# Optimization experiments

Hardware: AMD Instinct MI355X
Metric: run time of the kernel (lower is better)

The kernel has to match this reference:

```python
import jax, jax.numpy as jnp
from jax import lax
import numpy as np

VOCAB = 50000
EMBED = 300
UNITS = 512          # num_nodes[0]
D1 = 1024            # num_nodes[1]
D2 = 1024            # num_nodes[2]
NUM_CLASSES = 20
B, T = 64, 512


def setup_inputs() -> dict:
    key = jax.random.key(0)
    ks = jax.random.split(key, 12)
    s = 0.02
    return {
        "tokens": jax.random.randint(ks[0], (B, T), 0, VOCAB),
        "emb": jax.random.normal(ks[1], (VOCAB, EMBED), jnp.float32) * s,
        "Wx": jax.random.normal(ks[2], (EMBED, 4 * UNITS), jnp.float32) * s,
        "Wh": jax.random.normal(ks[3], (UNITS, 4 * UNITS), jnp.float32) * s,
        "b": jnp.zeros((4 * UNITS,), jnp.float32),
        "W1": jax.random.normal(ks[4], (UNITS, D1), jnp.float32) * s,
        "b1": jnp.zeros((D1,), jnp.float32),
        "W2": jax.random.normal(ks[5], (D1, D2), jnp.float32) * s,
        "b2": jnp.zeros((D2,), jnp.float32),
        "Wo": jax.random.normal(ks[6], (D2, NUM_CLASSES), jnp.float32) * s,
        "bo": jnp.zeros((NUM_CLASSES,), jnp.float32),
    }


def reference(tokens, emb, Wx, Wh, b, W1, b1, W2, b2, Wo, bo):
    # Embedding with mask_zero=True: token 0 timesteps are masked -> LSTM skips
    # the state update (Keras semantics).
    mask = (tokens != 0)                               # [B, T]
    x = emb[tokens]                                    # [B, T, E]
    units = Wh.shape[0]
    # Precompute input contribution to the gates (parallel over time).
    xg = jnp.einsum('bte,eg->btg', x, Wx) + b          # [B, T, 4U]

    def step(carry, inp):
        h, c = carry
        g_x, m = inp                                   # [B,4U], [B]
        g = g_x + h @ Wh                               # [B, 4U]
        i, f, cc, o = jnp.split(g, 4, axis=-1)         # Keras gate order i,f,c,o
        i = jax.nn.sigmoid(i)
        f = jax.nn.sigmoid(f)
        o = jax.nn.sigmoid(o)
        # activation='relu' replaces tanh in candidate and output transform.
        c_new = f * c + i * jax.nn.relu(cc)
        h_new = o * jax.nn.relu(c_new)
        m = m[:, None]
        h = jnp.where(m, h_new, h)
        c = jnp.where(m, c_new, c)
        return (h, c), None

    h0 = jnp.zeros((tokens.shape[0], units), x.dtype)
    (h, _), _ = lax.scan(step, (h0, h0),
                         (jnp.swapaxes(xg, 0, 1), mask.T))  # scan over T

    h = jax.nn.relu(h @ W1 + b1)
    h = jax.nn.relu(h @ W2 + b2)
    return jax.nn.softmax(h @ Wo + bo)
```

## Files before the change

### kernel.cpp

```cpp
#include <hip/hip_runtime.h>
#include <hip/hip_bf16.h>

#define B_   64
#define T_   512
#define E_   300
#define U_   512
#define G4_  2048
#define D1_  1024
#define D2_  1024
#define NC_  20
#define KP_  320

typedef __bf16 bf16x8 __attribute__((ext_vector_type(8)));
typedef float  f32x4  __attribute__((ext_vector_type(4)));

__device__ __forceinline__ float sigmoidf_(float x) { return 1.0f / (1.0f + __expf(-x)); }

__device__ __forceinline__ void gl_lds16(const void* g, void* l) {
    __builtin_amdgcn_global_load_lds(
        (const __attribute__((address_space(1))) unsigned int*)g,
        (__attribute__((address_space(3))) unsigned int*)l, 16, 0, 0);
}

__global__ void init_kernel(unsigned int* __restrict__ hz, int* __restrict__ flags) {
    int idx = blockIdx.x * 256 + threadIdx.x;
    if (idx < (B_ * U_ / 2)) hz[idx] = 0u;
    if (idx < 256) flags[idx] = 0;
}

__global__ __launch_bounds__(256) void prep_wxT(const float* __restrict__ Wx,
                                                __hip_bfloat16* __restrict__ wxT) {
    __shared__ __hip_bfloat16 t[64][65];
    const int n0 = blockIdx.x * 64;
    const int k0 = blockIdx.y * 64;
    const int tid = threadIdx.x;
    for (int i = tid; i < 4096; i += 256) {
        int r = i >> 6, c = i & 63;
        int k = k0 + r;
        float v = (k < E_) ? Wx[(size_t)k * G4_ + n0 + c] : 0.f;
        t[r][c] = __float2bfloat16(v);
    }
    __syncthreads();
    for (int i = tid; i < 4096; i += 256) {
        int r = i >> 6, c = i & 63;
        wxT[(size_t)(n0 + r) * KP_ + k0 + c] = t[c][r];
    }
}

__global__ __launch_bounds__(256) void prep_xb(const int* __restrict__ tokens,
                                               const float* __restrict__ emb,
                                               __hip_bfloat16* __restrict__ xb) {
    const int row = blockIdx.x * 4 + (threadIdx.x >> 6);
    const int ln  = threadIdx.x & 63;
    const int tok = tokens[row];
    const float* src = emb + (size_t)tok * E_;
    __hip_bfloat16* dst = xb + (size_t)row * KP_;
    for (int k = ln; k < KP_; k += 64)
        dst[k] = (k < E_) ? __float2bfloat16(src[k]) : __float2bfloat16(0.f);
}

__global__ __launch_bounds__(256) void xg_gemm(const __hip_bfloat16* __restrict__ xb,
                                               const __hip_bfloat16* __restrict__ wxT,
                                               const float* __restrict__ bias,
                                               __hip_bfloat16* __restrict__ xg) {
    const int n0g = blockIdx.x * 128;
    const int bt0 = blockIdx.y * 128;
    const int tid = threadIdx.x;
    const int w   = tid >> 6;
    const int ln  = tid & 63;
    const int fn  = ln & 15;
    const int quad = ln >> 4;
    const int m0  = (w >> 1) * 64;
    const int n0w = (w & 1) * 64;

    __shared__ __align__(16) __hip_bfloat16 As[128 * 32];
    __shared__ __align__(16) __hip_bfloat16 Bs[128 * 32];

    f32x4 acc[4][4];
    #pragma unroll
    for (int im = 0; im < 4; ++im)
        #pragma unroll
        for (int in = 0; in < 4; ++in)
            acc[im][in] = (f32x4){0.f, 0.f, 0.f, 0.f};

    const __hip_bfloat16* ga = xb  + (size_t)(bt0 + w * 32 + (ln >> 2)) * KP_ + (ln & 3) * 8;
    const __hip_bfloat16* gb = wxT + (size_t)(n0g + w * 32 + (ln >> 2)) * KP_ + (ln & 3) * 8;

    for (int kt = 0; kt < KP_ / 32; ++kt) {
        gl_lds16(ga,             &As[(w * 32) * 32]);
        gl_lds16(ga + 16 * KP_,  &As[(w * 32 + 16) * 32]);
        gl_lds16(gb,             &Bs[(w * 32) * 32]);
        gl_lds16(gb + 16 * KP_,  &Bs[(w * 32 + 16) * 32]);
        ga += 32; gb += 32;
        __syncthreads();

        bf16x8 af[4], bf[4];
        #pragma unroll
        for (int im = 0; im < 4; ++im)
            af[im] = *(const bf16x8*)&As[(m0 + im * 16 + fn) * 32 + quad * 8];
        #pragma unroll
        for (int in = 0; in < 4; ++in)
            bf[in] = *(const bf16x8*)&Bs[(n0w + in * 16 + fn) * 32 + quad * 8];
        #pragma unroll
        for (int im = 0; im < 4; ++im)
            #pragma unroll
            for (int in = 0; in < 4; ++in)
                acc[im][in] = __builtin_amdgcn_mfma_f32_16x16x32_bf16(
                    af[im], bf[in], acc[im][in], 0, 0, 0);
        __syncthreads();
    }

    #pragma unroll
    for (int in = 0; in < 4; ++in) {
        const int n = n0g + n0w + in * 16 + fn;
        const float bv = bias[n];
        #pragma unroll
        for (int im = 0; im < 4; ++im) {
            #pragma unroll
            for (int r = 0; r < 4; ++r) {
                int m = bt0 + m0 + im * 16 + quad * 4 + r;
                int bb = m >> 9, tt = m & 511;
                xg[(size_t)(tt * B_ + bb) * G4_ + n] =
                    __float2bfloat16(acc[im][in][r] + bv);
            }
        }
    }
}

__global__ __launch_bounds__(256) void lstm_kernel(const __hip_bfloat16* __restrict__ xg,
                                                   const int* __restrict__ tokens,
                                                   const float* __restrict__ Wh,
                                                   __hip_bfloat16* __restrict__ hbuf,
                                                   int* __restrict__ flags) {
    const int tid  = threadIdx.x;
    const int lane = tid & 63;
    const int wave = tid >> 6;
    const int x  = blockIdx.x & 7;
    const int r_ = blockIdx.x >> 3;
    const int ub = x * 8 + (r_ & 7);
    const int g  = r_ >> 3;
    const int u0 = ub * 8;

    __shared__ __align__(16) __hip_bfloat16 whsT[32][520];
    __shared__ __align__(16) __hip_bfloat16 hs[16][520];
    __shared__ float gbuf[16][32];
    __shared__ unsigned mask_lds[16][16];

    for (int idx = tid; idx < 32 * 512; idx += 256) {
        int c = idx & 31, k = idx >> 5;
        int col = ((c >> 3) << 9) + u0 + (c & 7);
        whsT[c][k] = __float2bfloat16(Wh[(size_t)k * G4_ + col]);
    }
    {
        int m = tid >> 4, wi = tid & 15;
        const int4* tp = (const int4*)(tokens + (size_t)(g * 16 + m) * T_ + wi * 32);
        unsigned bits = 0;
        #pragma unroll
        for (int q = 0; q < 8; ++q) {
            int4 v = tp[q];
            bits |= (v.x != 0 ? 1u : 0u) << (q * 4 + 0);
            bits |= (v.y != 0 ? 1u : 0u) << (q * 4 + 1);
            bits |= (v.z != 0 ? 1u : 0u) << (q * 4 + 2);
            bits |= (v.w != 0 ? 1u : 0u) << (q * 4 + 3);
        }
        mask_lds[m][wi] = bits;
    }

    float c0 = 0.f, c1 = 0.f, h0 = 0.f, h1 = 0.f;
    int* gflags = flags + g * 64;

    const int fn   = lane & 15;
    const int quad = lane >> 4;
    const int fc   = wave * 16 + fn;
    const int fcol = ((fc >> 3) << 9) + u0 + (fc & 7);

    __syncthreads();

    for (int s = 0; s < T_; ++s) {
        float xv[4];
        if (wave < 2) {
            #pragma unroll
            for (int r = 0; r < 4; ++r)
                xv[r] = __bfloat162float(
                    xg[(size_t)(s * B_ + g * 16 + quad * 4 + r) * G4_ + fcol]);
        }

        if (s > 0) {
            if (tid < 64) {
                while (__hip_atomic_load(&gflags[tid], __ATOMIC_RELAXED,
                                         __HIP_MEMORY_SCOPE_AGENT) < s)
                    __builtin_amdgcn_s_sleep(2);
            }
            __syncthreads();
        }

        {
            const uint4* hp = (const uint4*)(hbuf + (size_t)((s & 1) * B_ + g * 16) * U_);
            uint4 t0, t1, t2, t3;
            asm volatile(
                "global_load_dwordx4 %0, %4, off sc0 sc1\n\t"
                "global_load_dwordx4 %1, %5, off sc0 sc1\n\t"
                "global_load_dwordx4 %2, %6, off sc0 sc1\n\t"
                "s_waitcnt vmcnt(0)\n\t"
                "global_load_dwordx4 %3, %7, off sc0 sc1\n\t"
                "s_waitcnt vmcnt(0)"
                : "=&v"(t0), "=&v"(t1), "=&v"(t2), "=&v"(t3)
                : "v"(hp + tid), "v"(hp + tid + 256), "v"(hp + tid + 512),
                  "v"(hp + tid + 768)
                : "memory");
            int i0 = tid;        *((uint4*)&hs[i0 >> 6][(i0 & 63) * 8]) = t0;
            int i1 = tid + 256;  *((uint4*)&hs[i1 >> 6][(i1 & 63) * 8]) = t1;
            int i2 = tid + 512;  *((uint4*)&hs[i2 >> 6][(i2 & 63) * 8]) = t2;
            int i3 = tid + 768;  *((uint4*)&hs[i3 >> 6][(i3 & 63) * 8]) = t3;
        }
        __syncthreads();

        if (wave < 2) {
            f32x4 acc;
            #pragma unroll
            for (int r = 0; r < 4; ++r) acc[r] = xv[r];
            const __hip_bfloat16* arow = &hs[fn][quad * 8];
            const __hip_bfloat16* brow = &whsT[fc][quad * 8];
            #pragma unroll
            for (int kk = 0; kk < 16; ++kk) {
                bf16x8 av = *(const bf16x8*)(arow + kk * 32);
                bf16x8 bv = *(const bf16x8*)(brow + kk * 32);
                acc = __builtin_amdgcn_mfma_f32_16x16x32_bf16(av, bv, acc, 0, 0, 0);
            }
            #pragma unroll
            for (int r = 0; r < 4; ++r)
                gbuf[quad * 4 + r][fc] = acc[r];
        }
        __syncthreads();

        if (tid < 64) {
            const int m  = tid >> 2;
            const int u2 = (tid & 3) << 1;
            float gi0 = sigmoidf_(gbuf[m][u2]),      gi1 = sigmoidf_(gbuf[m][u2 + 1]);
            float gf0 = sigmoidf_(gbuf[m][8 + u2]),  gf1 = sigmoidf_(gbuf[m][9 + u2]);
            float gc0 = gbuf[m][16 + u2],            gc1 = gbuf[m][17 + u2];
            float go0 = sigmoidf_(gbuf[m][24 + u2]), go1 = sigmoidf_(gbuf[m][25 + u2]);
            float cn0 = gf0 * c0 + gi0 * fmaxf(gc0, 0.f);
            float cn1 = gf1 * c1 + gi1 * fmaxf(gc1, 0.f);
            float hn0 = go0 * fmaxf(cn0, 0.f);
            float hn1 = go1 * fmaxf(cn1, 0.f);
            if ((mask_lds[m][s >> 5] >> (s & 31)) & 1u) {
                c0 = cn0; c1 = cn1; h0 = hn0; h1 = hn1;
            }
            __hip_bfloat162 hv;
            hv.x = __float2bfloat16(h0);
            hv.y = __float2bfloat16(h1);
            unsigned wv;
            __builtin_memcpy(&wv, &hv, 4);
            unsigned* dst = (unsigned*)hbuf +
                (((((s + 1) & 1) * B_ + g * 16 + m) * U_ + u0 + u2) >> 1);
            __hip_atomic_store(dst, wv, __ATOMIC_RELAXED, __HIP_MEMORY_SCOPE_AGENT);
        }
        __syncthreads();
        if (tid == 0)
            __hip_atomic_store(&gflags[ub], s + 1, __ATOMIC_RELAXED,
                               __HIP_MEMORY_SCOPE_AGENT);
    }
}

__global__ __launch_bounds__(256) void fc1_kernel(const __hip_bfloat16* __restrict__ h,
                                                  const float* __restrict__ W,
                                                  const float* __restrict__ bias,
                                                  float* __restrict__ y) {
    int b = blockIdx.x >> 2, ch = blockIdx.x & 3;
    __shared__ float xrow[U_];
    for (int i = threadIdx.x; i < U_; i += 256)
        xrow[i] = __bfloat162float(h[b * U_ + i]);
    __syncthreads();
    int n = ch * 256 + threadIdx.x;
    float acc = 0.f;
    #pragma unroll 4
    for (int k = 0; k < U_; ++k) acc = fmaf(xrow[k], W[(size_t)k * D1_ + n], acc);
    y[b * D1_ + n] = fmaxf(acc + bias[n], 0.f);
}

__global__ __launch_bounds__(256) void fc2_kernel(const float* __restrict__ x,
                                                  const float* __restrict__ W,
                                                  const float* __restrict__ bias,
                                                  float* __restrict__ y) {
    int b = blockIdx.x >> 2, ch = blockIdx.x & 3;
    __shared__ float xrow[D1_];
    for (int i = threadIdx.x; i < D1_; i += 256) xrow[i] = x[b * D1_ + i];
    __syncthreads();
    int n = ch * 256 + threadIdx.x;
    float acc = 0.f;
    #pragma unroll 4
    for (int k = 0; k < D1_; ++k) acc = fmaf(xrow[k], W[(size_t)k * D2_ + n], acc);
    y[b * D2_ + n] = fmaxf(acc + bias[n], 0.f);
}

__global__ __launch_bounds__(64) void out_kernel(const float* __restrict__ h2,
                                                 const float* __restrict__ Wo,
                                                 const float* __restrict__ bo,
                                                 float* __restrict__ out) {
    int b = blockIdx.x;
    __shared__ float xrow[D2_];
    __shared__ float lg[NC_];
    __shared__ float red[2];
    for (int i = threadIdx.x; i < D2_; i += 64) xrow[i] = h2[b * D2_ + i];
    __syncthreads();
    if (threadIdx.x < NC_) {
        float a = bo[threadIdx.x];
        for (int k = 0; k < D2_; ++k) a = fmaf(xrow[k], Wo[k * NC_ + threadIdx.x], a);
        lg[threadIdx.x] = a;
    }
    __syncthreads();
    if (threadIdx.x == 0) {
        float mx = lg[0];
        for (int c = 1; c < NC_; ++c) mx = fmaxf(mx, lg[c]);
        float sm = 0.f;
        for (int c = 0; c < NC_; ++c) sm += expf(lg[c] - mx);
        red[0] = mx; red[1] = 1.0f / sm;
    }
    __syncthreads();
    if (threadIdx.x < NC_)
        out[b * NC_ + threadIdx.x] = expf(lg[threadIdx.x] - red[0]) * red[1];
}

extern "C" void kernel_launch(void* const* d_in, const int* in_sizes, int n_in,
                              void* d_out, int out_size, void* d_ws, size_t ws_size,
                              hipStream_t stream) {
    const int*   tokens = (const int*)d_in[0];
    const float* emb    = (const float*)d_in[1];
    const float* Wx     = (const float*)d_in[2];
    const float* Wh     = (const float*)d_in[3];
    const float* b      = (const float*)d_in[4];
    const float* W1     = (const float*)d_in[5];
    const float* b1     = (const float*)d_in[6];
    const float* W2     = (const float*)d_in[7];
    const float* b2     = (const float*)d_in[8];
    const float* Wo     = (const float*)d_in[9];
    const float* bo     = (const float*)d_in[10];
    float* out = (float*)d_out;

    char* ws = (char*)d_ws;
    const size_t XG_BYTES   = (size_t)T_ * B_ * G4_ * 2;
    const size_t HBUF_BYTES = (size_t)2 * B_ * U_ * 2;
    __hip_bfloat16* xg   = (__hip_bfloat16*)ws;
    __hip_bfloat16* hbuf = (__hip_bfloat16*)(ws + XG_BYTES);
    int* flags           = (int*)(ws + XG_BYTES + HBUF_BYTES);
    char* p = ws + XG_BYTES + HBUF_BYTES + 1024;
    float* h1            = (float*)p;                 p += (size_t)B_ * D1_ * 4;
    float* h2            = (float*)p;                 p += (size_t)B_ * D2_ * 4;
    __hip_bfloat16* xb   = (__hip_bfloat16*)p;        p += (size_t)B_ * T_ * KP_ * 2;
    __hip_bfloat16* wxT  = (__hip_bfloat16*)p;

    init_kernel<<<64, 256, 0, stream>>>((unsigned int*)hbuf, flags);
    prep_wxT<<<dim3(32, 5), 256, 0, stream>>>(Wx, wxT);
    prep_xb<<<(B_ * T_) / 4, 256, 0, stream>>>(tokens, emb, xb);
    xg_gemm<<<dim3(16, 256), 256, 0, stream>>>(xb, wxT, b, xg);
    lstm_kernel<<<256, 256, 0, stream>>>(xg, tokens, Wh, hbuf, flags);
    fc1_kernel<<<256, 256, 0, stream>>>(hbuf, W1, b1, h1);
    fc2_kernel<<<256, 256, 0, stream>>>(h1, W2, b2, h2);
    out_kernel<<<64, 64, 0, stream>>>(h2, Wo, bo, out);
}
```

Before: 1.643 ms.

## Drop per-step block barriers in persistent LSTM and split MFMA accumulator chain

Each step now has every wave poll the inter-block flags itself, instead of one wave polling and then a block barrier. The trailing barrier before the flag publish is removed: wave 0 waits for its own h stores with s_waitcnt and then sets the flag directly. The h-load asm no longer waits between loads, and the 16-deep MFMA dependency chain is split into two independent accumulators that are summed at the end. The aim is to shorten per-step latency on the serial recurrence. The cost is more polling traffic, and correctness now depends on the flag ordering alone to protect the shared-memory buffers.

After: 2.025 ms. +23.2%, slower.

```diff
diff --git a/kernel.cpp b/kernel.cpp
--- a/kernel.cpp
+++ b/kernel.cpp
@@ -168,12 +168,16 @@
 
     float c0 = 0.f, c1 = 0.f, h0 = 0.f, h1 = 0.f;
     int* gflags = flags + g * 64;
+    volatile int* myflag = gflags + (tid & 63);
 
     const int fn   = lane & 15;
     const int quad = lane >> 4;
     const int fc   = wave * 16 + fn;
     const int fcol = ((fc >> 3) << 9) + u0 + (fc & 7);
 
+    const uint4* hp0 = (const uint4*)(hbuf + (size_t)(g * 16) * U_) + tid;
+    const uint4* hp1 = (const uint4*)(hbuf + (size_t)(B_ + g * 16) * U_) + tid;
+
     __syncthreads();
 
     for (int s = 0; s < T_; ++s) {
@@ -186,27 +190,22 @@
         }
 
         if (s > 0) {
-            if (tid < 64) {
-                while (__hip_atomic_load(&gflags[tid], __ATOMIC_RELAXED,
-                                         __HIP_MEMORY_SCOPE_AGENT) < s)
-                    __builtin_amdgcn_s_sleep(2);
-            }
-            __syncthreads();
+            while (__hip_atomic_load(&gflags[tid & 63], __ATOMIC_RELAXED,
+                                     __HIP_MEMORY_SCOPE_AGENT) < s)
+                __builtin_amdgcn_s_sleep(1);
         }
 
         {
-            const uint4* hp = (const uint4*)(hbuf + (size_t)((s & 1) * B_ + g * 16) * U_);
+            const uint4* hp = (s & 1) ? hp1 : hp0;
             uint4 t0, t1, t2, t3;
             asm volatile(
                 "global_load_dwordx4 %0, %4, off sc0 sc1\n\t"
                 "global_load_dwordx4 %1, %5, off sc0 sc1\n\t"
                 "global_load_dwordx4 %2, %6, off sc0 sc1\n\t"
-                "s_waitcnt vmcnt(0)\n\t"
                 "global_load_dwordx4 %3, %7, off sc0 sc1\n\t"
                 "s_waitcnt vmcnt(0)"
                 : "=&v"(t0), "=&v"(t1), "=&v"(t2), "=&v"(t3)
-                : "v"(hp + tid), "v"(hp + tid + 256), "v"(hp + tid + 512),
-                  "v"(hp + tid + 768)
+                : "v"(hp), "v"(hp + 256), "v"(hp + 512), "v"(hp + 768)
                 : "memory");
             int i0 = tid;        *((uint4*)&hs[i0 >> 6][(i0 & 63) * 8]) = t0;
             int i1 = tid + 256;  *((uint4*)&hs[i1 >> 6][(i1 & 63) * 8]) = t1;
@@ -216,20 +215,23 @@
         __syncthreads();
 
         if (wave < 2) {
-            f32x4 acc;
-            #pragma unroll
-            for (int r = 0; r < 4; ++r) acc[r] = xv[r];
+            f32x4 acc0, acc1;
+            #pragma unroll
+            for (int r = 0; r < 4; ++r) { acc0[r] = xv[r]; acc1[r] = 0.f; }
             const __hip_bfloat16* arow = &hs[fn][quad * 8];
             const __hip_bfloat16* brow = &whsT[fc][quad * 8];
             #pragma unroll
-            for (int kk = 0; kk < 16; ++kk) {
-                bf16x8 av = *(const bf16x8*)(arow + kk * 32);
-                bf16x8 bv = *(const bf16x8*)(brow + kk * 32);
-                acc = __builtin_amdgcn_mfma_f32_16x16x32_bf16(av, bv, acc, 0, 0, 0);
+            for (int kk = 0; kk < 8; ++kk) {
+                bf16x8 av0 = *(const bf16x8*)(arow + kk * 32);
+                bf16x8 bv0 = *(const bf16x8*)(brow + kk * 32);
+                acc0 = __builtin_amdgcn_mfma_f32_16x16x32_bf16(av0, bv0, acc0, 0, 0, 0);
+                bf16x8 av1 = *(const bf16x8*)(arow + (kk + 8) * 32);
+                bf16x8 bv1 = *(const bf16x8*)(brow + (kk + 8) * 32);
+                acc1 = __builtin_amdgcn_mfma_f32_16x16x32_bf16(av1, bv1, acc1, 0, 0, 0);
             }
             #pragma unroll
             for (int r = 0; r < 4; ++r)
-                gbuf[quad * 4 + r][fc] = acc[r];
+                gbuf[quad * 4 + r][fc] = acc0[r] + acc1[r];
         }
         __syncthreads();
 
@@ -255,12 +257,13 @@
             unsigned* dst = (unsigned*)hbuf +
                 (((((s + 1) & 1) * B_ + g * 16 + m) * U_ + u0 + u2) >> 1);
             __hip_atomic_store(dst, wv, __ATOMIC_RELAXED, __HIP_MEMORY_SCOPE_AGENT);
-        }
-        __syncthreads();
-        if (tid == 0)
-            __hip_atomic_store(&gflags[ub], s + 1, __ATOMIC_RELAXED,
-                               __HIP_MEMORY_SCOPE_AGENT);
-    }
+            asm volatile("s_waitcnt vmcnt(0)" ::: "memory");
+            if (tid == 0)
+                __hip_atomic_store(&gflags[ub], s + 1, __ATOMIC_RELAXED,
+                                   __HIP_MEMORY_SCOPE_AGENT);
+        }
+    }
+    (void)myflag;
 }
 
 __global__ __launch_bounds__(256) void fc1_kernel(const __hip_bfloat16* __restrict__ h,
```

## Replace per-step flag barrier with step-tagged hidden-state words and prefetch xg

Applied to the files above, without the earlier changes.

The per-block completion flags and the spin-wait on them are removed. Each hidden-state bf16 pair is now stored alongside its step number in one 8-byte word. Readers load the state directly and retry any 16-byte chunk whose tags do not match the current step. This removes the separate flag poll and one __syncthreads per step, and the input-gate values for step s+1 are prefetched during step s. In exchange the hidden-state buffer doubles in size, spinning becomes per-chunk, and correctness now depends on each 8-byte store being seen as a single unit.

Result: slower. 2.568 ms (+56.2%).

```diff
diff --git a/kernel.cpp b/kernel.cpp
--- a/kernel.cpp
+++ b/kernel.cpp
@@ -22,10 +22,16 @@
         (__attribute__((address_space(3))) unsigned int*)l, 16, 0, 0);
 }
 
-__global__ void init_kernel(unsigned int* __restrict__ hz, int* __restrict__ flags) {
+__device__ __forceinline__ uint4 cload4(const uint4* p) {
+    uint4 t;
+    asm volatile("global_load_dwordx4 %0, %1, off sc0 sc1\n\ts_waitcnt vmcnt(0)"
+                 : "=v"(t) : "v"(p) : "memory");
+    return t;
+}
+
+__global__ void init_kernel(uint4* __restrict__ hz) {
     int idx = blockIdx.x * 256 + threadIdx.x;
-    if (idx < (B_ * U_ / 2)) hz[idx] = 0u;
-    if (idx < 256) flags[idx] = 0;
+    hz[idx] = (uint4){0u, 0u, 0u, 0u};
 }
 
 __global__ __launch_bounds__(256) void prep_wxT(const float* __restrict__ Wx,
@@ -130,8 +136,7 @@
 __global__ __launch_bounds__(256) void lstm_kernel(const __hip_bfloat16* __restrict__ xg,
                                                    const int* __restrict__ tokens,
                                                    const float* __restrict__ Wh,
-                                                   __hip_bfloat16* __restrict__ hbuf,
-                                                   int* __restrict__ flags) {
+                                                   uint2* __restrict__ hbuf2) {
     const int tid  = threadIdx.x;
     const int lane = tid & 63;
     const int wave = tid >> 6;
@@ -167,7 +172,6 @@
     }
 
     float c0 = 0.f, c1 = 0.f, h0 = 0.f, h1 = 0.f;
-    int* gflags = flags + g * 64;
 
     const int fn   = lane & 15;
     const int quad = lane >> 4;
@@ -176,44 +180,65 @@
 
     __syncthreads();
 
+    float xvp[4];
+    if (wave < 2) {
+        #pragma unroll
+        for (int r = 0; r < 4; ++r)
+            xvp[r] = __bfloat162float(
+                xg[(size_t)(0 * B_ + g * 16 + quad * 4 + r) * G4_ + fcol]);
+    }
+
     for (int s = 0; s < T_; ++s) {
         float xv[4];
         if (wave < 2) {
             #pragma unroll
+            for (int r = 0; r < 4; ++r) xv[r] = xvp[r];
+        }
+
+        {
+            const uint4* hp = (const uint4*)(hbuf2 +
+                (size_t)((s & 1) * (B_ * 256) + (g * 16) * 256)) + tid;
+            uint4 t0, t1, t2, t3, t4, t5, t6, t7;
+            asm volatile(
+                "global_load_dwordx4 %0, %8,  off sc0 sc1\n\t"
+                "global_load_dwordx4 %1, %9,  off sc0 sc1\n\t"
+                "global_load_dwordx4 %2, %10, off sc0 sc1\n\t"
+                "global_load_dwordx4 %3, %11, off sc0 sc1\n\t"
+                "global_load_dwordx4 %4, %12, off sc0 sc1\n\t"
+                "global_load_dwordx4 %5, %13, off sc0 sc1\n\t"
+                "global_load_dwordx4 %6, %14, off sc0 sc1\n\t"
+                "global_load_dwordx4 %7, %15, off sc0 sc1\n\t"
+                "s_waitcnt vmcnt(0)"
+                : "=&v"(t0), "=&v"(t1), "=&v"(t2), "=&v"(t3),
+                  "=&v"(t4), "=&v"(t5), "=&v"(t6), "=&v"(t7)
+                : "v"(hp), "v"(hp + 256), "v"(hp + 512), "v"(hp + 768),
+                  "v"(hp + 1024), "v"(hp + 1280), "v"(hp + 1536), "v"(hp + 1792)
+                : "memory");
+
+            const unsigned tgt = (unsigned)s;
+            #define RETRY_(tt, pp) \
+                while (tt.y != tgt || tt.w != tgt) { \
+                    __builtin_amdgcn_s_sleep(1); tt = cload4(pp); }
+            RETRY_(t0, hp);        RETRY_(t1, hp + 256);
+            RETRY_(t2, hp + 512);  RETRY_(t3, hp + 768);
+            RETRY_(t4, hp + 1024); RETRY_(t5, hp + 1280);
+            RETRY_(t6, hp + 1536); RETRY_(t7, hp + 1792);
+            #undef RETRY_
+
+            #define HSW_(tt, k) { int u = tid + 256 * (k); \
+                *(uint2*)&hs[u >> 7][(u & 127) * 4] = (uint2){tt.x, tt.z}; }
+            HSW_(t0, 0) HSW_(t1, 1) HSW_(t2, 2) HSW_(t3, 3)
+            HSW_(t4, 4) HSW_(t5, 5) HSW_(t6, 6) HSW_(t7, 7)
+            #undef HSW_
+        }
+        __syncthreads();
+
+        if (wave < 2 && s + 1 < T_) {
+            #pragma unroll
             for (int r = 0; r < 4; ++r)
-                xv[r] = __bfloat162float(
-                    xg[(size_t)(s * B_ + g * 16 + quad * 4 + r) * G4_ + fcol]);
-        }
-
-        if (s > 0) {
-            if (tid < 64) {
-                while (__hip_atomic_load(&gflags[tid], __ATOMIC_RELAXED,
-                                         __HIP_MEMORY_SCOPE_AGENT) < s)
-                    __builtin_amdgcn_s_sleep(2);
-            }
-            __syncthreads();
-        }
-
-        {
-            const uint4* hp = (const uint4*)(hbuf + (size_t)((s & 1) * B_ + g * 16) * U_);
-            uint4 t0, t1, t2, t3;
-            asm volatile(
-                "global_load_dwordx4 %0, %4, off sc0 sc1\n\t"
-                "global_load_dwordx4 %1, %5, off sc0 sc1\n\t"
-                "global_load_dwordx4 %2, %6, off sc0 sc1\n\t"
-                "s_waitcnt vmcnt(0)\n\t"
-                "global_load_dwordx4 %3, %7, off sc0 sc1\n\t"
-                "s_waitcnt vmcnt(0)"
-                : "=&v"(t0), "=&v"(t1), "=&v"(t2), "=&v"(t3)
-                : "v"(hp + tid), "v"(hp + tid + 256), "v"(hp + tid + 512),
-                  "v"(hp + tid + 768)
-                : "memory");
-            int i0 = tid;        *((uint4*)&hs[i0 >> 6][(i0 & 63) * 8]) = t0;
-            int i1 = tid + 256;  *((uint4*)&hs[i1 >> 6][(i1 & 63) * 8]) = t1;
-            int i2 = tid + 512;  *((uint4*)&hs[i2 >> 6][(i2 & 63) * 8]) = t2;
-            int i3 = tid + 768;  *((uint4*)&hs[i3 >> 6][(i3 & 63) * 8]) = t3;
-        }
-        __syncthreads();
+                xvp[r] = __bfloat162float(
+                    xg[(size_t)((s + 1) * B_ + g * 16 + quad * 4 + r) * G4_ + fcol]);
+        }
 
         if (wave < 2) {
             f32x4 acc;
@@ -252,25 +277,29 @@
             hv.y = __float2bfloat16(h1);
             unsigned wv;
             __builtin_memcpy(&wv, &hv, 4);
-            unsigned* dst = (unsigned*)hbuf +
-                (((((s + 1) & 1) * B_ + g * 16 + m) * U_ + u0 + u2) >> 1);
-            __hip_atomic_store(dst, wv, __ATOMIC_RELAXED, __HIP_MEMORY_SCOPE_AGENT);
-        }
-        __syncthreads();
-        if (tid == 0)
-            __hip_atomic_store(&gflags[ub], s + 1, __ATOMIC_RELAXED,
-                               __HIP_MEMORY_SCOPE_AGENT);
-    }
-}
-
-__global__ __launch_bounds__(256) void fc1_kernel(const __hip_bfloat16* __restrict__ h,
+            uint2 val; val.x = wv; val.y = (unsigned)(s + 1);
+            uint2* dst = hbuf2 + (size_t)(((s + 1) & 1) * (B_ * 256) +
+                                          (g * 16 + m) * 256 + ub * 4 + (tid & 3));
+            asm volatile("global_store_dwordx2 %0, %1, off sc0 sc1"
+                         :: "v"(dst), "v"(val) : "memory");
+        }
+        __builtin_amdgcn_s_barrier();
+    }
+}
+
+__global__ __launch_bounds__(256) void fc1_kernel(const uint2* __restrict__ hb2,
                                                   const float* __restrict__ W,
                                                   const float* __restrict__ bias,
                                                   float* __restrict__ y) {
     int b = blockIdx.x >> 2, ch = blockIdx.x & 3;
     __shared__ float xrow[U_];
-    for (int i = threadIdx.x; i < U_; i += 256)
-        xrow[i] = __bfloat162float(h[b * U_ + i]);
+    for (int i = threadIdx.x; i < U_ / 2; i += 256) {
+        uint2 v = hb2[(size_t)b * 256 + i];
+        __hip_bfloat162 hv;
+        __builtin_memcpy(&hv, &v.x, 4);
+        xrow[2 * i]     = __bfloat162float(hv.x);
+        xrow[2 * i + 1] = __bfloat162float(hv.y);
+    }
     __syncthreads();
     int n = ch * 256 + threadIdx.x;
     float acc = 0.f;
@@ -340,22 +369,21 @@
 
     char* ws = (char*)d_ws;
     const size_t XG_BYTES   = (size_t)T_ * B_ * G4_ * 2;
-    const size_t HBUF_BYTES = (size_t)2 * B_ * U_ * 2;
-    __hip_bfloat16* xg   = (__hip_bfloat16*)ws;
-    __hip_bfloat16* hbuf = (__hip_bfloat16*)(ws + XG_BYTES);
-    int* flags           = (int*)(ws + XG_BYTES + HBUF_BYTES);
-    char* p = ws + XG_BYTES + HBUF_BYTES + 1024;
+    const size_t HB2_BYTES  = (size_t)2 * B_ * 256 * 8;
+    __hip_bfloat16* xg  = (__hip_bfloat16*)ws;
+    uint2* hbuf2        = (uint2*)(ws + XG_BYTES);
+    char* p = ws + XG_BYTES + HB2_BYTES;
     float* h1            = (float*)p;                 p += (size_t)B_ * D1_ * 4;
     float* h2            = (float*)p;                 p += (size_t)B_ * D2_ * 4;
     __hip_bfloat16* xb   = (__hip_bfloat16*)p;        p += (size_t)B_ * T_ * KP_ * 2;
     __hip_bfloat16* wxT  = (__hip_bfloat16*)p;
 
-    init_kernel<<<64, 256, 0, stream>>>((unsigned int*)hbuf, flags);
+    init_kernel<<<64, 256, 0, stream>>>((uint4*)hbuf2);
     prep_wxT<<<dim3(32, 5), 256, 0, stream>>>(Wx, wxT);
     prep_xb<<<(B_ * T_) / 4, 256, 0, stream>>>(tokens, emb, xb);
     xg_gemm<<<dim3(16, 256), 256, 0, stream>>>(xb, wxT, b, xg);
-    lstm_kernel<<<256, 256, 0, stream>>>(xg, tokens, Wh, hbuf, flags);
-    fc1_kernel<<<256, 256, 0, stream>>>(hbuf, W1, b1, h1);
+    lstm_kernel<<<256, 256, 0, stream>>>(xg, tokens, Wh, hbuf2);
+    fc1_kernel<<<256, 256, 0, stream>>>(hbuf2, W1, b1, h1);
     fc2_kernel<<<256, 256, 0, stream>>>(h1, W2, b2, h2);
     out_kernel<<<64, 64, 0, stream>>>(h2, Wo, bo, out);
 }
```

## Compute LSTM cell in registers via shuffles and publish per-wave flags

Applied to the files above, without the earlier changes.

Reorders the recurrent weight columns so each wave's MFMA tile holds all four gates for four units, then combines gates with lane shuffles instead of an LDS gate buffer. The cell update runs in the MFMA waves, and each wave stores its h values and signals its own flag right away. This removes two block barriers and an LDS round trip from every serial timestep. In exchange, consumers poll twice as many flags and h is written with narrower stores.

After: 2.127 ms. 29.4% more time.

```diff
diff --git a/kernel.cpp b/kernel.cpp
--- a/kernel.cpp
+++ b/kernel.cpp
@@ -25,7 +25,7 @@
 __global__ void init_kernel(unsigned int* __restrict__ hz, int* __restrict__ flags) {
     int idx = blockIdx.x * 256 + threadIdx.x;
     if (idx < (B_ * U_ / 2)) hz[idx] = 0u;
-    if (idx < 256) flags[idx] = 0;
+    if (idx < 512) flags[idx] = 0;
 }
 
 __global__ __launch_bounds__(256) void prep_wxT(const float* __restrict__ Wx,
@@ -143,12 +143,11 @@
 
     __shared__ __align__(16) __hip_bfloat16 whsT[32][520];
     __shared__ __align__(16) __hip_bfloat16 hs[16][520];
-    __shared__ float gbuf[16][32];
     __shared__ unsigned mask_lds[16][16];
 
     for (int idx = tid; idx < 32 * 512; idx += 256) {
         int c = idx & 31, k = idx >> 5;
-        int col = ((c >> 3) << 9) + u0 + (c & 7);
+        int col = (((c >> 2) & 3) << 9) + u0 + ((c >> 4) << 2) + (c & 3);
         whsT[c][k] = __float2bfloat16(Wh[(size_t)k * G4_ + col]);
     }
     {
@@ -166,13 +165,15 @@
         mask_lds[m][wi] = bits;
     }
 
-    float c0 = 0.f, c1 = 0.f, h0 = 0.f, h1 = 0.f;
-    int* gflags = flags + g * 64;
+    float cst[4] = {0.f, 0.f, 0.f, 0.f};
+    float hst[4] = {0.f, 0.f, 0.f, 0.f};
+    int* gfl = flags + g * 128;
 
     const int fn   = lane & 15;
     const int quad = lane >> 4;
-    const int fc   = wave * 16 + fn;
-    const int fcol = ((fc >> 3) << 9) + u0 + (fc & 7);
+    const int gate = fn >> 2;
+    const int uloc = (wave << 2) + (fn & 3);
+    const int fcol = (gate << 9) + u0 + uloc;
 
     __syncthreads();
 
@@ -186,8 +187,8 @@
         }
 
         if (s > 0) {
-            if (tid < 64) {
-                while (__hip_atomic_load(&gflags[tid], __ATOMIC_RELAXED,
+            if (tid < 128) {
+                while (__hip_atomic_load(&gfl[tid], __ATOMIC_RELAXED,
                                          __HIP_MEMORY_SCOPE_AGENT) < s)
                     __builtin_amdgcn_s_sleep(2);
             }
@@ -220,46 +221,51 @@
             #pragma unroll
             for (int r = 0; r < 4; ++r) acc[r] = xv[r];
             const __hip_bfloat16* arow = &hs[fn][quad * 8];
-            const __hip_bfloat16* brow = &whsT[fc][quad * 8];
+            const __hip_bfloat16* brow = &whsT[wave * 16 + fn][quad * 8];
             #pragma unroll
             for (int kk = 0; kk < 16; ++kk) {
                 bf16x8 av = *(const bf16x8*)(arow + kk * 32);
                 bf16x8 bv = *(const bf16x8*)(brow + kk * 32);
                 acc = __builtin_amdgcn_mfma_f32_16x16x32_bf16(av, bv, acc, 0, 0, 0);
             }
-            #pragma unroll
-            for (int r = 0; r < 4; ++r)
-                gbuf[quad * 4 + r][fc] = acc[r];
-        }
-        __syncthreads();
-
-        if (tid < 64) {
-            const int m  = tid >> 2;
-            const int u2 = (tid & 3) << 1;
-            float gi0 = sigmoidf_(gbuf[m][u2]),      gi1 = sigmoidf_(gbuf[m][u2 + 1]);
-            float gf0 = sigmoidf_(gbuf[m][8 + u2]),  gf1 = sigmoidf_(gbuf[m][9 + u2]);
-            float gc0 = gbuf[m][16 + u2],            gc1 = gbuf[m][17 + u2];
-            float go0 = sigmoidf_(gbuf[m][24 + u2]), go1 = sigmoidf_(gbuf[m][25 + u2]);
-            float cn0 = gf0 * c0 + gi0 * fmaxf(gc0, 0.f);
-            float cn1 = gf1 * c1 + gi1 * fmaxf(gc1, 0.f);
-            float hn0 = go0 * fmaxf(cn0, 0.f);
-            float hn1 = go1 * fmaxf(cn1, 0.f);
-            if ((mask_lds[m][s >> 5] >> (s & 31)) & 1u) {
-                c0 = cn0; c1 = cn1; h0 = hn0; h1 = hn1;
-            }
-            __hip_bfloat162 hv;
-            hv.x = __float2bfloat16(h0);
-            hv.y = __float2bfloat16(h1);
-            unsigned wv;
-            __builtin_memcpy(&wv, &hv, 4);
-            unsigned* dst = (unsigned*)hbuf +
-                (((((s + 1) & 1) * B_ + g * 16 + m) * U_ + u0 + u2) >> 1);
-            __hip_atomic_store(dst, wv, __ATOMIC_RELAXED, __HIP_MEMORY_SCOPE_AGENT);
-        }
-        __syncthreads();
-        if (tid == 0)
-            __hip_atomic_store(&gflags[ub], s + 1, __ATOMIC_RELAXED,
-                               __HIP_MEMORY_SCOPE_AGENT);
+
+            float p1[4], p2[4], p3[4];
+            #pragma unroll
+            for (int r = 0; r < 4; ++r) p1[r] = __shfl_xor(acc[r], 4);
+            #pragma unroll
+            for (int r = 0; r < 4; ++r) p2[r] = __shfl_xor(acc[r], 8);
+            #pragma unroll
+            for (int r = 0; r < 4; ++r) p3[r] = __shfl_xor(p1[r], 8);
+
+            if (gate == 0) {
+                #pragma unroll
+                for (int r = 0; r < 4; ++r) {
+                    const int m = quad * 4 + r;
+                    float iv = sigmoidf_(acc[r]);
+                    float fv = sigmoidf_(p1[r]);
+                    float cc = p2[r];
+                    float ov = sigmoidf_(p3[r]);
+                    float cn = fv * cst[r] + iv * fmaxf(cc, 0.f);
+                    float hn = ov * fmaxf(cn, 0.f);
+                    if ((mask_lds[m][s >> 5] >> (s & 31)) & 1u) {
+                        cst[r] = cn; hst[r] = hn;
+                    }
+                    __hip_bfloat16 hb = __float2bfloat16(hst[r]);
+                    unsigned hv = 0;
+                    __builtin_memcpy(&hv, &hb, 2);
+                    __hip_bfloat16* dst = hbuf +
+                        (size_t)(((s + 1) & 1) * B_ + g * 16 + m) * U_ + u0 + uloc;
+                    asm volatile("global_store_short %0, %1, off sc0 sc1"
+                                 :: "v"(dst), "v"(hv) : "memory");
+                }
+            }
+            asm volatile("s_waitcnt vmcnt(0)" ::: "memory");
+            if (lane == 0) {
+                unsigned sv = (unsigned)(s + 1);
+                asm volatile("global_store_dword %0, %1, off sc0 sc1"
+                             :: "v"(&gfl[wave * 64 + ub]), "v"(sv) : "memory");
+            }
+        }
     }
 }
 
@@ -344,7 +350,7 @@
     __hip_bfloat16* xg   = (__hip_bfloat16*)ws;
     __hip_bfloat16* hbuf = (__hip_bfloat16*)(ws + XG_BYTES);
     int* flags           = (int*)(ws + XG_BYTES + HBUF_BYTES);
-    char* p = ws + XG_BYTES + HBUF_BYTES + 1024;
+    char* p = ws + XG_BYTES + HBUF_BYTES + 4096;
     float* h1            = (float*)p;                 p += (size_t)B_ * D1_ * 4;
     float* h2            = (float*)p;                 p += (size_t)B_ * D2_ * 4;
     __hip_bfloat16* xb   = (__hip_bfloat16*)p;        p += (size_t)B_ * T_ * KP_ * 2;
```
